# Optimization experiments

Hardware: AMD Instinct MI355X
Metric: run time of the kernel (lower is better)

Reference implementation:

```python
import jax, jax.numpy as jnp
import numpy as np

N_QUBITS = 10
DEPTH = 5
DIM = 2 ** N_QUBITS  # 1024
NUM_CLASSES = 2
BATCH = 16384
IN_DIM = 784


def _rot_matrices(w):
    # w: [depth, n_qubits, 3] angles (phi, theta, omega); qml.Rot = RZ(omega) RY(theta) RZ(phi)
    phi, theta, omega = w[..., 0], w[..., 1], w[..., 2]
    c, s = jnp.cos(theta / 2), jnp.sin(theta / 2)
    e = lambda a: jnp.exp(1j * a.astype(jnp.complex64))
    m00 = e(-(phi + omega) / 2) * c
    m01 = -e((phi - omega) / 2) * s
    m10 = e(-(phi - omega) / 2) * s
    m11 = e((phi + omega) / 2) * c
    return jnp.stack([jnp.stack([m00, m01], -1), jnp.stack([m10, m11], -1)], -2)  # [D, n, 2, 2]


def _apply_1q(state, U, w):
    # state: [B] + [2]*n ; apply 2x2 U on qubit axis w
    s = jnp.moveaxis(state, w + 1, -1)
    s = s @ U.T
    return jnp.moveaxis(s, -1, w + 1)


def _apply_cnot(state, c, t):
    s = jnp.moveaxis(state, (c + 1, t + 1), (-2, -1))
    s = jnp.concatenate([s[..., 0:1, :], s[..., 1:2, ::-1]], axis=-2)  # flip target where control=1
    return jnp.moveaxis(s, (-2, -1), (c + 1, t + 1))


def _circuit(x, weights):
    B = x.shape[0]
    # AmplitudeEmbedding: pad_with=0, normalize=True
    amp = jnp.pad(x, ((0, 0), (0, DIM - x.shape[1])))
    amp = amp / jnp.linalg.norm(amp, axis=1, keepdims=True)
    state = amp.astype(jnp.complex64).reshape((B,) + (2,) * N_QUBITS)
    U = _rot_matrices(weights)
    for d in range(DEPTH):
        for i in range(N_QUBITS):  # entangling CNOT ring
            state = _apply_cnot(state, i, (i + 1) % N_QUBITS)
        for i in range(N_QUBITS):  # per-qubit Rot
            state = _apply_1q(state, U[d, i], i)
    probs = (state.real ** 2 + state.imag ** 2).reshape(B, DIM)
    # <Z_i> = P(bit_i = 0) - P(bit_i = 1)
    z = []
    for i in range(N_QUBITS):
        p = probs.reshape(B, 2 ** i, 2, -1)
        z.append(p[:, :, 0, :].sum((1, 2)) - p[:, :, 1, :].sum((1, 2)))
    return jnp.stack(z, axis=1)  # [B, n_qubits]


def setup_inputs() -> dict:
    key = jax.random.key(0)
    k1, k2, k3 = jax.random.split(key, 3)
    x = jax.random.normal(k1, (BATCH, IN_DIM), dtype=jnp.float32)
    weights = jax.random.uniform(k2, (DEPTH, N_QUBITS, 3), dtype=jnp.float32) * (2.0 * np.pi)
    y = jax.random.randint(k3, (BATCH,), 0, NUM_CLASSES)
    return {"x": x, "weights": weights, "y": y}


def reference(x, weights, y):
    logits = _circuit(x, weights)[:, :NUM_CLASSES]
    logp = jax.nn.log_softmax(logits, axis=-1)
    loss = -jnp.take_along_axis(logp, y[:, None], axis=1).mean()
    return loss
```

## Files before the change

### kernel.cpp

```cpp
#include <hip/hip_runtime.h>
#include <type_traits>

#define NQ 10
#define N_DEPTH 5
#define DIM 1024
#define BATCH 16384
#define IN_DIM 784
#define NGATES 50
#define KALLOC 832
#define NT 13
#define NSLOT 768
#define NB 12

typedef float f32x2 __attribute__((ext_vector_type(2)));
typedef float f32x4 __attribute__((ext_vector_type(4)));
typedef unsigned u32x4 __attribute__((ext_vector_type(4)));

struct MaskTab {
  unsigned v[NGATES];
  unsigned p[NGATES];
  unsigned vz0, vz1;
};

constexpr MaskTab make_masks() {
  MaskTab t{};
  unsigned v[NQ], p[NQ];
  for (int i = 0; i < NQ; ++i) { v[i] = 1u << (9 - i); p[i] = 1u << (9 - i); }
  for (int d = 0; d < N_DEPTH; ++d) {
    for (int i = 0; i < NQ; ++i) {
      int c = i, tt = (i + 1) % NQ;
      v[tt] ^= v[c];
      p[c]  ^= p[tt];
    }
    for (int i = 0; i < NQ; ++i) {
      t.v[d * NQ + i] = v[i];
      t.p[d * NQ + i] = p[i];
    }
  }
  t.vz0 = v[0];
  t.vz1 = v[1];
  return t;
}

constexpr MaskTab MT = make_masks();
__constant__ MaskTab d_MT = make_masks();

struct PermTab { short slot[DIM]; };
constexpr PermTab make_perm() {
  PermTab t{};
  int a = 0, b = 256, c = 512;
  for (int m = 0; m < DIM; ++m) {
    const int p0 = __builtin_popcount((unsigned)m & MT.vz0) & 1;
    const int p1 = __builtin_popcount((unsigned)m & MT.vz1) & 1;
    if (p0 && !p1)      t.slot[m] = (short)a++;
    else if (!p0 && p1) t.slot[m] = (short)b++;
    else if (p0 && p1)  t.slot[m] = (short)c++;
    else                t.slot[m] = -1;
  }
  return t;
}
__constant__ PermTab d_PT = make_perm();

__device__ __forceinline__ f32x2 ampfma(f32x2 o, f32x2 q, f32x2 co, f32x2 cp) {
  f32x2 d;
  asm("v_pk_mul_f32 %0, %2, %1 op_sel:[0,0] op_sel_hi:[0,1]\n\t"
      "v_pk_fma_f32 %0, %2, %1, %0 op_sel:[1,1,0] op_sel_hi:[1,0,1] neg_lo:[1,0,0]\n\t"
      "v_pk_fma_f32 %0, %3, %4, %0 op_sel:[0,0,0] op_sel_hi:[0,1,1]\n\t"
      "v_pk_fma_f32 %0, %3, %4, %0 op_sel:[1,1,0] op_sel_hi:[1,0,1] neg_lo:[1,0,0]"
      : "=&v"(d)
      : "v"(o), "v"(co), "v"(cp), "v"(q));
  return d;
}

__device__ __forceinline__ float fxor(float x, unsigned m) {
  return __uint_as_float(__float_as_uint(x) ^ m);
}

__device__ __forceinline__ unsigned pk4_fp8(float a, float b, float c, float d) {
  int v = __builtin_amdgcn_cvt_pk_fp8_f32(a, b, 0, false);
  v = __builtin_amdgcn_cvt_pk_fp8_f32(c, d, v, true);
  return (unsigned)v;
}

__device__ __forceinline__ void gll16(const void* g, void* l) {
  __builtin_amdgcn_global_load_lds(
      (const __attribute__((address_space(1))) void*)g,
      (__attribute__((address_space(3))) void*)l, 16, 0, 0);
}

#define XSCALE 32.0f
#define WSCALE 16.0f
#define SINV   (1.0f / 262144.0f)

__global__ __launch_bounds__(256) void prep(const float* __restrict__ X,
                                            char* __restrict__ Xf8,
                                            float* __restrict__ xn2,
                                            const float* __restrict__ w,
                                            unsigned short* __restrict__ W2u) {
  __shared__ f32x4 UL4[NGATES];
  __shared__ f32x2 S0[DIM];
  __shared__ f32x2 S1[DIM];

  const int tid = threadIdx.x;

  if (blockIdx.x >= 832) {
    const int row = (blockIdx.x - 832) * 8 + (tid >> 5);
    const int l32 = tid & 31;
    const float* src = X + (size_t)row * IN_DIM;
    char* dst = Xf8 + (size_t)row * KALLOC;
    float ssq = 0.0f;
    for (int c = l32; c < 52; c += 32) {
      u32x4 out;
      if (c < 49) {
        f32x4 v0 = *(const f32x4*)(src + c * 16);
        f32x4 v1 = *(const f32x4*)(src + c * 16 + 4);
        f32x4 v2 = *(const f32x4*)(src + c * 16 + 8);
        f32x4 v3 = *(const f32x4*)(src + c * 16 + 12);
        ssq += v0.x * v0.x + v0.y * v0.y + v0.z * v0.z + v0.w * v0.w +
               v1.x * v1.x + v1.y * v1.y + v1.z * v1.z + v1.w * v1.w +
               v2.x * v2.x + v2.y * v2.y + v2.z * v2.z + v2.w * v2.w +
               v3.x * v3.x + v3.y * v3.y + v3.z * v3.z + v3.w * v3.w;
        out = u32x4{
          pk4_fp8(v0.x * XSCALE, v0.y * XSCALE, v0.z * XSCALE, v0.w * XSCALE),
          pk4_fp8(v1.x * XSCALE, v1.y * XSCALE, v1.z * XSCALE, v1.w * XSCALE),
          pk4_fp8(v2.x * XSCALE, v2.y * XSCALE, v2.z * XSCALE, v2.w * XSCALE),
          pk4_fp8(v3.x * XSCALE, v3.y * XSCALE, v3.z * XSCALE, v3.w * XSCALE)};
      } else {
        out = u32x4{0, 0, 0, 0};
      }
      *(u32x4*)(dst + c * 16) = out;
    }
#pragma unroll
    for (int off = 1; off < 32; off <<= 1) ssq += __shfl_xor(ssq, off);
    if (l32 == 0) xn2[row] = ssq;
    return;
  }

  if (tid < NGATES) {
    float phi = w[tid * 3 + 0], th = w[tid * 3 + 1], om = w[tid * 3 + 2];
    float ct = cosf(th * 0.5f), st = sinf(th * 0.5f);
    float aa = (phi + om) * 0.5f, bb = (phi - om) * 0.5f;
    float cA = cosf(aa), sA = sinf(aa), cB = cosf(bb), sB = sinf(bb);
    UL4[tid] = f32x4{ ct * cA, -ct * sA, -st * cB, -st * sB };
  }

  const int j = blockIdx.x;
  unsigned short* rowp = W2u + (size_t)j * NSLOT;

  if (j >= IN_DIM) {
#pragma unroll
    for (int k = 0; k < 3; ++k) rowp[tid + k * 256] = 0;
    return;
  }

#pragma unroll
  for (int k = 0; k < 4; ++k) {
    const int m = tid + k * 256;
    S0[m] = f32x2{(m == j) ? 1.0f : 0.0f, 0.0f};
  }
  __syncthreads();

  for (int g = 0; g < NGATES; ++g) {
    const f32x2* src = (g & 1) ? S1 : S0;
    f32x2* dst = (g & 1) ? S0 : S1;
    const f32x4 A = UL4[g];
    const unsigned v = d_MT.v[g];
    const unsigned p = d_MT.p[g];
#pragma unroll
    for (int k = 0; k < 4; ++k) {
      const int m = tid + k * 256;
      f32x2 o = src[m];
      f32x2 q = src[m ^ (int)p];
      const unsigned sg = (unsigned)(__popc((int)((unsigned)m & v)) & 1) << 31;
      const f32x2 co = {A.x, fxor(A.y, sg)};
      const f32x2 cp = {fxor(A.z, sg), A.w};
      dst[m] = ampfma(o, q, co, cp);
    }
    __syncthreads();
  }

  const f32x2* fin = S0;
#pragma unroll
  for (int k = 0; k < 4; ++k) {
    const int m = tid + k * 256;
    const int s = d_PT.slot[m];
    f32x2 a = fin[m];
    if (s >= 0)
      rowp[s] = (unsigned short)(pk4_fp8(a.x * WSCALE, a.y * WSCALE,
                                         0.0f, 0.0f) & 0xffffu);
  }
}

__global__ __launch_bounds__(256) void transpose_w(const unsigned* __restrict__ W2u32,
                                                   unsigned* __restrict__ W2Tu32) {
  __shared__ unsigned tile[64][33];
  const int j0 = blockIdx.x * 64;
  const int s0 = blockIdx.y * 64;
  const int t = threadIdx.x;
#pragma unroll
  for (int i = 0; i < 8; ++i) {
    const int idx = i * 256 + t;
    const int jr = idx >> 5, sc = idx & 31;
    tile[jr][sc] = W2u32[(size_t)(j0 + jr) * (NSLOT / 2) + (s0 >> 1) + sc];
  }
  __syncthreads();
#pragma unroll
  for (int i = 0; i < 8; ++i) {
    const int idx = i * 256 + t;
    const int rl = idx >> 4, jq = idx & 15;
    const int slot = rl >> 1, c = rl & 1;
    const int sc = slot >> 1, p = slot & 1;
    unsigned out = 0;
#pragma unroll
    for (int q = 0; q < 4; ++q) {
      const unsigned w32 = tile[jq * 4 + q][sc];
      const unsigned h = (w32 >> (16 * p)) & 0xffffu;
      out |= ((h >> (8 * c)) & 0xffu) << (8 * q);
    }
    const int orow = 2 * (s0 + slot) + c;
    W2Tu32[((size_t)orow * KALLOC + j0 + jq * 4) >> 2] = out;
  }
}

__global__ __launch_bounds__(512) void gemm_fused(const char* __restrict__ Xf8,
                                                  const char* __restrict__ W2T,
                                                  float* __restrict__ accb) {
  __shared__ u32x4 lds4[3072];
  char* lds = (char*)lds4;

  const int tid = threadIdx.x;
  const int orig = blockIdx.x;
  const int bx = (orig & 7) * 96 + (orig >> 3);
  const int mb = bx / NB, nb = bx % NB;
  const int m0 = mb * 256, n0 = nb * 128;
  const int lane = tid & 63, wv = tid >> 6;
  const int wm = wv >> 2, wn = wv & 3;

  const int rl = lane >> 2;
  const int csrc = (lane & 3) ^ (rl & 3) ^ ((rl >> 2) & 3);

  auto stage = [&](int t) {
    char* Ab = lds + (t & 1) * 24576;
    char* Bb = Ab + 16384;
    const int col = t * 64 + csrc * 16;
#pragma unroll
    for (int i = 0; i < 2; ++i) {
      const int g = wv * 2 + i;
      const int row = g * 16 + rl;
      gll16(Xf8 + (size_t)(m0 + row) * KALLOC + col, Ab + g * 1024);
    }
    {
      const int row = wv * 16 + rl;
      gll16(W2T + (size_t)(n0 + row) * KALLOC + col, Bb + wv * 1024);
    }
  };

  stage(0);
  asm volatile("s_waitcnt vmcnt(0)" ::: "memory");
  __builtin_amdgcn_s_barrier();

  f32x4 acc[8][2];
#pragma unroll
  for (int fm = 0; fm < 8; ++fm)
#pragma unroll
    for (int fn = 0; fn < 2; ++fn) acc[fm][fn] = f32x4{0, 0, 0, 0};

  const int kc = lane >> 4;

  for (int t = 0; t < NT; ++t) {
    const char* Ab = lds + (t & 1) * 24576;
    const char* Bb = Ab + 16384;

    long af0[8], bf0[2], af1[8], bf1[2];
#pragma unroll
    for (int f = 0; f < 8; ++f) {
      const int ar = wm * 128 + f * 16 + (lane & 15);
      const int sw = (ar & 3) ^ ((ar >> 2) & 3);
      af0[f] = *(const long*)(Ab + ar * 64 + (((kc >> 1) ^ sw) * 16) + (kc & 1) * 8);
    }
#pragma unroll
    for (int f = 0; f < 2; ++f) {
      const int br = wn * 32 + f * 16 + (lane & 15);
      const int sw = (br & 3) ^ ((br >> 2) & 3);
      bf0[f] = *(const long*)(Bb + br * 64 + (((kc >> 1) ^ sw) * 16) + (kc & 1) * 8);
    }
    if (t < NT - 1) stage(t + 1);
#pragma unroll
    for (int f = 0; f < 8; ++f) {
      const int ar = wm * 128 + f * 16 + (lane & 15);
      const int sw = (ar & 3) ^ ((ar >> 2) & 3);
      const int kb = 4 + kc;
      af1[f] = *(const long*)(Ab + ar * 64 + (((kb >> 1) ^ sw) * 16) + (kb & 1) * 8);
    }
#pragma unroll
    for (int f = 0; f < 2; ++f) {
      const int br = wn * 32 + f * 16 + (lane & 15);
      const int sw = (br & 3) ^ ((br >> 2) & 3);
      const int kb = 4 + kc;
      bf1[f] = *(const long*)(Bb + br * 64 + (((kb >> 1) ^ sw) * 16) + (kb & 1) * 8);
    }

    __builtin_amdgcn_s_setprio(1);
#pragma unroll
    for (int fm = 0; fm < 8; ++fm)
#pragma unroll
      for (int fn = 0; fn < 2; ++fn)
        acc[fm][fn] = __builtin_amdgcn_mfma_f32_16x16x32_fp8_fp8(
            af0[fm], bf0[fn], acc[fm][fn], 0, 0, 0);
    __builtin_amdgcn_s_setprio(0);

    __builtin_amdgcn_s_setprio(1);
#pragma unroll
    for (int fm = 0; fm < 8; ++fm)
#pragma unroll
      for (int fn = 0; fn < 2; ++fn)
        acc[fm][fn] = __builtin_amdgcn_mfma_f32_16x16x32_fp8_fp8(
            af1[fm], bf1[fn], acc[fm][fn], 0, 0, 0);
    __builtin_amdgcn_s_setprio(0);

    if (t < NT - 1) {
      asm volatile("s_waitcnt vmcnt(0)" ::: "memory");
      __builtin_amdgcn_sched_barrier(0);
      __builtin_amdgcn_s_barrier();
    }
  }

#pragma unroll
  for (int fm = 0; fm < 8; ++fm) {
    float sn[4] = {0, 0, 0, 0};
#pragma unroll
    for (int fn = 0; fn < 2; ++fn) {
#pragma unroll
      for (int r = 0; r < 4; ++r) {
        const float vv = acc[fm][fn][r];
        sn[r] = fmaf(vv, vv, sn[r]);
      }
    }
#pragma unroll
    for (int off = 1; off < 16; off <<= 1) {
#pragma unroll
      for (int r = 0; r < 4; ++r) sn[r] += __shfl_xor(sn[r], off);
    }
    if ((lane & 15) == 0) {
#pragma unroll
      for (int r = 0; r < 4; ++r) {
        const int m = m0 + wm * 128 + fm * 16 + (lane >> 4) * 4 + r;
        accb[(size_t)nb * BATCH + m] = sn[r];
      }
    }
  }
}

__global__ __launch_bounds__(256) void loss_partial(const float* __restrict__ accb,
                                                    const float* __restrict__ xn2,
                                                    const int* __restrict__ y,
                                                    float* __restrict__ partial) {
  const int s = blockIdx.x * 256 + threadIdx.x;
  float SA = 0.0f, SB = 0.0f, SC = 0.0f;
#pragma unroll
  for (int k = 0; k < 4; ++k) {
    SA += accb[(size_t)(0 + k) * BATCH + s];
    SB += accb[(size_t)(4 + k) * BATCH + s];
    SC += accb[(size_t)(8 + k) * BATCH + s];
  }
  SA *= SINV; SB *= SINV; SC *= SINV;
  const float n2 = xn2[s];
  const float z0 = n2 - 2.0f * (SA + SC);
  const float z1 = n2 - 2.0f * (SB + SC);
  const float inv = 1.0f / n2;
  const float l0 = z0 * inv, l1 = z1 * inv;
  const float mx = fmaxf(l0, l1);
  const float lse = mx + logf(expf(l0 - mx) + expf(l1 - mx));
  float loss = lse - ((y[s] == 0) ? l0 : l1);

  __shared__ float sm[256];
  sm[threadIdx.x] = loss;
  __syncthreads();
  for (int st = 128; st > 0; st >>= 1) {
    if (threadIdx.x < st) sm[threadIdx.x] += sm[threadIdx.x + st];
    __syncthreads();
  }
  if (threadIdx.x == 0) partial[blockIdx.x] = sm[0];
}

__global__ __launch_bounds__(64) void loss_final(const float* __restrict__ partial,
                                                 float* __restrict__ out) {
  float v = partial[threadIdx.x];
#pragma unroll
  for (int off = 1; off < 64; off <<= 1) v += __shfl_xor(v, off);
  if (threadIdx.x == 0) out[0] = v * (1.0f / (float)BATCH);
}

extern "C" void kernel_launch(void* const* d_in, const int* in_sizes, int n_in,
                              void* d_out, int out_size, void* d_ws, size_t ws_size,
                              hipStream_t stream) {
  const float* x = (const float*)d_in[0];
  const float* w = (const float*)d_in[1];
  const int*   y = (const int*)d_in[2];

  char* ws = (char*)d_ws;
  char*     Xf8  = ws;
  unsigned short* W2u = (unsigned short*)(ws + 13631488);
  char*     W2Tu = ws + 14909440;
  float*    xn2  = (float*)(ws + 16187392);
  float*    accb = (float*)(ws + 16252928);
  float* partial = (float*)(ws + 17039360);

  prep<<<2880, 256, 0, stream>>>(x, Xf8, xn2, w, W2u);
  transpose_w<<<dim3(13, 12), 256, 0, stream>>>((const unsigned*)W2u,
                                                (unsigned*)W2Tu);
  gemm_fused<<<768, 512, 0, stream>>>(Xf8, W2Tu, accb);
  loss_partial<<<BATCH / 256, 256, 0, stream>>>(accb, xn2, y, partial);
  loss_final<<<1, 64, 0, stream>>>(partial, (float*)d_out);
}
```

Measured before the change: 80.46 us.

## Keep circuit-simulation state in registers with cross-lane exchanges instead of LDS ping-pong

The kernel that builds the per-input-row unitary response used to apply all 50 gates through shared-memory ping-pong buffers with a barrier after every gate. It now maps the 1024 amplitudes onto registers (4 per thread), choosing at compile time the two qubit bits assigned to wavefronts so that as few gates as possible cross wavefronts. Gates whose partner index lies within a wavefront use DPP, permlane swaps or shuffles, or register pairing, and only the cross-wave gates go through LDS with a barrier. The gate schedule is fully unrolled with compile-time masks, which adds code size and register pressure. This is a precompute kernel, so its share of total time may be small.

```diff
diff --git a/kernel.cpp b/kernel.cpp
--- a/kernel.cpp
+++ b/kernel.cpp
@@ -43,7 +43,6 @@
 }
 
 constexpr MaskTab MT = make_masks();
-__constant__ MaskTab d_MT = make_masks();
 
 struct PermTab { short slot[DIM]; };
 constexpr PermTab make_perm() {
@@ -60,6 +59,122 @@
   return t;
 }
 __constant__ PermTab d_PT = make_perm();
+
+struct BitPlan { int wpos[2]; int rpos[2]; int lpos[6]; unsigned wmask; };
+constexpr BitPlan make_plan() {
+  BitPlan bp{};
+  int bestc = 1000; unsigned best = 3;
+  for (int a = 0; a < NQ; ++a)
+    for (int b = a + 1; b < NQ; ++b) {
+      unsigned m = (1u << a) | (1u << b);
+      int c = 0;
+      for (int g = 0; g < NGATES; ++g) if (MT.p[g] & m) ++c;
+      if (c < bestc) { bestc = c; best = m; }
+    }
+  bp.wmask = best;
+  int rem[NQ]; int nr = 0, wi = 0;
+  for (int b = 0; b < NQ; ++b) {
+    if (best & (1u << b)) bp.wpos[wi++] = b;
+    else rem[nr++] = b;
+  }
+  for (int i = 0; i < 6; ++i) bp.lpos[i] = rem[i];
+  bp.rpos[0] = rem[6]; bp.rpos[1] = rem[7];
+  return bp;
+}
+constexpr BitPlan BP = make_plan();
+
+constexpr unsigned gath_l(unsigned p) {
+  unsigned r = 0;
+  for (int i = 0; i < 6; ++i) if (p & (1u << BP.lpos[i])) r |= 1u << i;
+  return r;
+}
+constexpr unsigned gath_r(unsigned p) {
+  unsigned r = 0;
+  for (int i = 0; i < 2; ++i) if (p & (1u << BP.rpos[i])) r |= 1u << i;
+  return r;
+}
+constexpr unsigned scat_r(unsigned x) {
+  return ((x & 1u) << BP.rpos[0]) | (((x >> 1) & 1u) << BP.rpos[1]);
+}
+constexpr int ncross_before(int g) {
+  int c = 0;
+  for (int i = 0; i < g; ++i) if (MT.p[i] & BP.wmask) ++c;
+  return c;
+}
+
+template <int I, int N, typename F>
+__device__ __forceinline__ void static_for(F&& f) {
+  if constexpr (I < N) {
+    f(std::integral_constant<int, I>{});
+    static_for<I + 1, N>(static_cast<F&&>(f));
+  }
+}
+
+constexpr int xcost(unsigned m) {
+  constexpr int t[16] = {0,1,1,1,2,2,2,1,1,2,2,2,2,2,2,1};
+  return t[m & 15u] + (((m >> 4) & 1u) ? 3 : 0) + (((m >> 5) & 1u) ? 3 : 0);
+}
+
+template <int CTRL>
+__device__ __forceinline__ float dppf(float x) {
+  int xi = (int)__float_as_uint(x);
+  return __uint_as_float(
+      (unsigned)__builtin_amdgcn_update_dpp(xi, xi, CTRL, 0xF, 0xF, false));
+}
+
+__device__ __forceinline__ float plswap16(float x) {
+  float a = x, b = x;
+  asm("s_nop 1\n\t"
+      "v_permlane16_swap_b32 %0, %1" : "+v"(a), "+v"(b));
+  return (a + b) - x;
+}
+__device__ __forceinline__ float plswap32(float x) {
+  float a = x, b = x;
+  asm("s_nop 1\n\t"
+      "v_permlane32_swap_b32 %0, %1" : "+v"(a), "+v"(b));
+  return (a + b) - x;
+}
+
+template <unsigned M>
+__device__ __forceinline__ float xlane_f(float x) {
+  float r = x;
+  constexpr unsigned m4 = M & 15u;
+  if constexpr (m4 == 1u)  r = dppf<0x0B1>(r);
+  else if constexpr (m4 == 2u)  r = dppf<0x04E>(r);
+  else if constexpr (m4 == 3u)  r = dppf<0x01B>(r);
+  else if constexpr (m4 == 4u)  { r = dppf<0x141>(r); r = dppf<0x01B>(r); }
+  else if constexpr (m4 == 5u)  { r = dppf<0x141>(r); r = dppf<0x04E>(r); }
+  else if constexpr (m4 == 6u)  { r = dppf<0x141>(r); r = dppf<0x0B1>(r); }
+  else if constexpr (m4 == 7u)  r = dppf<0x141>(r);
+  else if constexpr (m4 == 8u)  r = dppf<0x128>(r);
+  else if constexpr (m4 == 9u)  { r = dppf<0x128>(r); r = dppf<0x0B1>(r); }
+  else if constexpr (m4 == 10u) { r = dppf<0x128>(r); r = dppf<0x04E>(r); }
+  else if constexpr (m4 == 11u) { r = dppf<0x128>(r); r = dppf<0x01B>(r); }
+  else if constexpr (m4 == 12u) { r = dppf<0x140>(r); r = dppf<0x01B>(r); }
+  else if constexpr (m4 == 13u) { r = dppf<0x140>(r); r = dppf<0x04E>(r); }
+  else if constexpr (m4 == 14u) { r = dppf<0x140>(r); r = dppf<0x0B1>(r); }
+  else if constexpr (m4 == 15u) r = dppf<0x140>(r);
+  if constexpr ((M & 16u) != 0u) r = plswap16(r);
+  if constexpr ((M & 32u) != 0u) r = plswap32(r);
+  return r;
+}
+
+template <unsigned M>
+__device__ __forceinline__ f32x2 xchg(f32x2 v) {
+  if constexpr (M == 0u) {
+    return v;
+  } else if constexpr (xcost(M) >= 5) {
+    f32x2 r;
+    r.x = __shfl_xor(v.x, (int)M);
+    r.y = __shfl_xor(v.y, (int)M);
+    return r;
+  } else {
+    f32x2 r;
+    r.x = xlane_f<M>(v.x);
+    r.y = xlane_f<M>(v.y);
+    return r;
+  }
+}
 
 __device__ __forceinline__ f32x2 ampfma(f32x2 o, f32x2 q, f32x2 co, f32x2 cp) {
   f32x2 d;
@@ -153,42 +268,98 @@
     return;
   }
 
-#pragma unroll
-  for (int k = 0; k < 4; ++k) {
-    const int m = tid + k * 256;
-    S0[m] = f32x2{(m == j) ? 1.0f : 0.0f, 0.0f};
-  }
+  const int wv = tid >> 6, lane = tid & 63;
+  unsigned mbase = ((unsigned)(wv & 1) << BP.wpos[0]) |
+                   ((unsigned)(wv >> 1) << BP.wpos[1]);
+#pragma unroll
+  for (int i = 0; i < 6; ++i)
+    mbase |= (((unsigned)lane >> i) & 1u) << BP.lpos[i];
+
+  f32x2 a[4];
+  static_for<0, 4>([&](auto R_) {
+    constexpr int r = decltype(R_)::value;
+    constexpr unsigned rs = scat_r((unsigned)r);
+    a[r] = f32x2{((mbase | rs) == (unsigned)j) ? 1.0f : 0.0f, 0.0f};
+  });
   __syncthreads();
 
-  for (int g = 0; g < NGATES; ++g) {
-    const f32x2* src = (g & 1) ? S1 : S0;
-    f32x2* dst = (g & 1) ? S0 : S1;
-    const f32x4 A = UL4[g];
-    const unsigned v = d_MT.v[g];
-    const unsigned p = d_MT.p[g];
-#pragma unroll
-    for (int k = 0; k < 4; ++k) {
-      const int m = tid + k * 256;
-      f32x2 o = src[m];
-      f32x2 q = src[m ^ (int)p];
-      const unsigned sg = (unsigned)(__popc((int)((unsigned)m & v)) & 1) << 31;
-      const f32x2 co = {A.x, fxor(A.y, sg)};
-      const f32x2 cp = {fxor(A.z, sg), A.w};
-      dst[m] = ampfma(o, q, co, cp);
-    }
-    __syncthreads();
-  }
-
-  const f32x2* fin = S0;
-#pragma unroll
-  for (int k = 0; k < 4; ++k) {
-    const int m = tid + k * 256;
+  static_for<0, NGATES>([&](auto G_) {
+    constexpr int G = decltype(G_)::value;
+    constexpr unsigned p = MT.p[G];
+    constexpr unsigned v = MT.v[G];
+    constexpr unsigned pw = p & BP.wmask;
+    const f32x4 A = UL4[G];
+
+    if constexpr (pw == 0u) {
+      constexpr unsigned lx = gath_l(p);
+      constexpr unsigned rx = gath_r(p);
+      if constexpr (rx == 0u) {
+        static_for<0, 4>([&](auto R_) {
+          constexpr int r = decltype(R_)::value;
+          constexpr unsigned rs = scat_r((unsigned)r);
+          f32x2 o = a[r];
+          f32x2 q = xchg<lx>(o);
+          const unsigned sg =
+              (unsigned)(__popc((int)((mbase | rs) & v)) & 1) << 31;
+          const f32x2 co = {A.x, fxor(A.y, sg)};
+          const f32x2 cp = {fxor(A.z, sg), A.w};
+          a[r] = ampfma(o, q, co, cp);
+        });
+      } else {
+        static_for<0, 4>([&](auto R_) {
+          constexpr int r = decltype(R_)::value;
+          constexpr int r2 = r ^ (int)rx;
+          if constexpr (r < r2) {
+            constexpr unsigned rs0 = scat_r((unsigned)r);
+            constexpr unsigned rs1 = scat_r((unsigned)r2);
+            f32x2 o0 = a[r], o1 = a[r2];
+            f32x2 q0 = xchg<lx>(o1);
+            f32x2 q1 = xchg<lx>(o0);
+            const unsigned sg0 =
+                (unsigned)(__popc((int)((mbase | rs0) & v)) & 1) << 31;
+            const unsigned sg1 =
+                (unsigned)(__popc((int)((mbase | rs1) & v)) & 1) << 31;
+            const f32x2 co0 = {A.x, fxor(A.y, sg0)};
+            const f32x2 cp0 = {fxor(A.z, sg0), A.w};
+            const f32x2 co1 = {A.x, fxor(A.y, sg1)};
+            const f32x2 cp1 = {fxor(A.z, sg1), A.w};
+            a[r]  = ampfma(o0, q0, co0, cp0);
+            a[r2] = ampfma(o1, q1, co1, cp1);
+          }
+        });
+      }
+    } else {
+      constexpr int cidx = ncross_before(G);
+      f32x2* S = (cidx & 1) ? S1 : S0;
+      static_for<0, 4>([&](auto R_) {
+        constexpr int r = decltype(R_)::value;
+        constexpr unsigned rs = scat_r((unsigned)r);
+        S[mbase | rs] = a[r];
+      });
+      __syncthreads();
+      static_for<0, 4>([&](auto R_) {
+        constexpr int r = decltype(R_)::value;
+        constexpr unsigned rs = scat_r((unsigned)r);
+        const unsigned m = mbase | rs;
+        f32x2 o = a[r];
+        f32x2 q = S[m ^ p];
+        const unsigned sg = (unsigned)(__popc((int)(m & v)) & 1) << 31;
+        const f32x2 co = {A.x, fxor(A.y, sg)};
+        const f32x2 cp = {fxor(A.z, sg), A.w};
+        a[r] = ampfma(o, q, co, cp);
+      });
+    }
+  });
+
+  static_for<0, 4>([&](auto R_) {
+    constexpr int r = decltype(R_)::value;
+    constexpr unsigned rs = scat_r((unsigned)r);
+    const unsigned m = mbase | rs;
     const int s = d_PT.slot[m];
-    f32x2 a = fin[m];
     if (s >= 0)
-      rowp[s] = (unsigned short)(pk4_fp8(a.x * WSCALE, a.y * WSCALE,
+      rowp[s] = (unsigned short)(pk4_fp8(a[r].x * WSCALE, a[r].y * WSCALE,
                                          0.0f, 0.0f) & 0xffffu);
-  }
+  });
 }
 
 __global__ __launch_bounds__(256) void transpose_w(const unsigned* __restrict__ W2u32,
```

Result: faster. 77.10 us, median of 2 (-4.2%).
